# Kernel optimization log

Hardware: AMD Instinct MI355X
Metric: run time of the kernel (lower is better)

## Reference

```python
import jax, jax.numpy as jnp
import numpy as np

B, N, D = 2, 1024, 128
MID, OUT = 128, 128
DE, DG = 16, 64
MLP_SIZES = [32, 64, 64, OUT]  # hardcoded in the original module


def _lin_init(key, fan_in, fan_out):
    s = 1.0 / np.sqrt(fan_in)
    return jax.random.uniform(key, (fan_in, fan_out), jnp.float32, -s, s)


def setup_inputs() -> dict:
    key = jax.random.key(0)
    ks = jax.random.split(key, 16)
    inp = {
        "features": jax.random.normal(ks[0], (B, N, D), jnp.float32),
        "e_features": jax.random.normal(ks[1], (B, N, N, DE), jnp.float32),
        "g_features": jax.random.normal(ks[2], (B, DG), jnp.float32),
        "adj": (jax.random.uniform(ks[3], (B, N, N)) < 0.5).astype(jnp.float32),
        # message linears m_1, m_2 : D -> MID
        "w1": _lin_init(ks[4], D, MID), "b1": jnp.zeros((MID,), jnp.float32),
        "w2": _lin_init(ks[5], D, MID), "b2": jnp.zeros((MID,), jnp.float32),
        # output linear o1 : D -> OUT
        "wo": _lin_init(ks[6], D, OUT), "bo": jnp.zeros((OUT,), jnp.float32),
    }
    # MLP([32,64,64,OUT]) acting on MID-dim msgs
    sizes = [MID] + MLP_SIZES
    for i in range(4):
        inp[f"wm{i}"] = _lin_init(ks[7 + i], sizes[i], sizes[i + 1])
        inp[f"bm{i}"] = jnp.zeros((sizes[i + 1],), jnp.float32)
    return inp


def reference(features, e_features, g_features, adj,
              w1, b1, w2, b2, wo, bo,
              wm0, bm0, wm1, bm1, wm2, bm2, wm3, bm3):
    # e_features and g_features are shape-checked but unused by the original.
    msg_1 = features @ w1 + b1                      # (b, n, mid)
    msg_2 = features @ w2 + b2                      # (b, n, mid)
    # all-pairs broadcast-add: (b,1,n,mid) + (b,n,1,mid) -> (b,n,n,mid)
    msgs = msg_1[:, None, :, :] + msg_2[:, :, None, :]
    # masked max-reduce over sender axis (axis=1), default reduction=jnp.max
    msgs = jnp.max(msgs * adj[..., None], axis=1)   # (b, n, mid)
    h_1 = features @ wo + bo                        # (b, n, out)
    # hk.nets.MLP([32,64,64,out]): relu between layers, none at the end
    x = jax.nn.relu(msgs)
    x = jax.nn.relu(x @ wm0 + bm0)
    x = jax.nn.relu(x @ wm1 + bm1)
    x = jax.nn.relu(x @ wm2 + bm2)
    h_2 = x @ wm3 + bm3                             # (b, n, out)
    return h_1 + h_2
```

## Files before the change

kernel.cpp:

```cpp
#include <hip/hip_runtime.h>

#define NN 1024
#define NROWS 2048

#define NEG_INF (-__builtin_huge_valf())

__device__ __forceinline__ float orf(float v, unsigned int m) {
    return __uint_as_float(__float_as_uint(v) | m);
}

__global__ __launch_bounds__(256) void k1_msg2(
    const float* __restrict__ feat, const float* __restrict__ w2,
    const float* __restrict__ b2, float* __restrict__ msg2)
{
    __shared__ float sf[4][128];
    const int tid = threadIdx.x;
    const int rb = blockIdx.x * 4;
    if (tid < 128) {
        int r = tid >> 5, c = (tid & 31) * 4;
        *reinterpret_cast<float4*>(&sf[r][c]) =
            *reinterpret_cast<const float4*>(feat + (size_t)(rb + r)*128 + c);
    }
    __syncthreads();
    const int m = tid & 127, rh = tid >> 7;
    float a0 = 0.f, a1 = 0.f;
    #pragma unroll 4
    for (int k = 0; k < 128; ++k) {
        float wv = w2[k*128 + m];
        a0 = fmaf(sf[rh*2][k],   wv, a0);
        a1 = fmaf(sf[rh*2+1][k], wv, a1);
    }
    const float bb = b2[m];
    msg2[(size_t)(rb + rh*2)*128 + m]     = a0 + bb;
    msg2[(size_t)(rb + rh*2 + 1)*128 + m] = a1 + bb;
}

struct K2S {
    union {
        float scratch[8][16][132];
        struct { float sf[8][128];
                 float sx[8][128];
                 float sh0[8][32]; float sh1[8][64]; float sh2[8][64]; } c;
    } u;
    unsigned long long adjm[128];
    float m1[8][128];
    float hh[8][128];
};

__global__ __launch_bounds__(512) void k2_fused(
    const float* __restrict__ feat, const float* __restrict__ adj,
    const float* __restrict__ msg2,
    const float* __restrict__ w1, const float* __restrict__ b1,
    const float* __restrict__ wo, const float* __restrict__ bo,
    const float* __restrict__ wm0, const float* __restrict__ bm0,
    const float* __restrict__ wm1, const float* __restrict__ bm1,
    const float* __restrict__ wm2, const float* __restrict__ bm2,
    const float* __restrict__ wm3, const float* __restrict__ bm3,
    float* __restrict__ out)
{
    __shared__ K2S sh;
    const int tid = threadIdx.x;
    const int orig = (blockIdx.x & 7) * 32 + (blockIdx.x >> 3);
    const int b  = orig >> 7;
    const int j0 = (orig & 127) * 8;
    const int rb = b * NN + j0;

    if (tid < 256) {
        int r = tid >> 5, c = (tid & 31) * 4;
        *reinterpret_cast<float4*>(&sh.u.c.sf[r][c]) =
            *reinterpret_cast<const float4*>(feat + (size_t)(rb + r)*128 + c);
    }
    const float* ga = adj + (size_t)b*NN*NN + j0;
    float av[16];
    #pragma unroll
    for (int k = 0; k < 16; ++k) {
        int e = tid + k*512;
        av[k] = ga[(size_t)(e >> 3)*NN + (e & 7)];
    }
    __syncthreads();

    {
        const int m = tid & 127, rr = tid >> 7;
        float a1v[2] = {0,0}, aov[2] = {0,0};
        #pragma unroll 4
        for (int k = 0; k < 128; ++k) {
            float wv1 = w1[k*128 + m], wvo = wo[k*128 + m];
            #pragma unroll
            for (int r = 0; r < 2; ++r) {
                float f = sh.u.c.sf[rr*2 + r][k];
                a1v[r] = fmaf(f, wv1, a1v[r]);
                aov[r] = fmaf(f, wvo, aov[r]);
            }
        }
        const float bb1 = b1[m], bbo = bo[m];
        #pragma unroll
        for (int r = 0; r < 2; ++r) {
            sh.m1[rr*2 + r][m] = a1v[r] + bb1;
            sh.hh[rr*2 + r][m] = aov[r] + bbo;
        }
    }
    #pragma unroll
    for (int k = 0; k < 16; ++k) {
        unsigned long long bal = __ballot(av[k] != 0.f);
        if ((tid & 63) == 0) sh.adjm[(tid + k*512) >> 6] = bal;
    }
    __syncthreads();

    const int mq = tid & 31;
    const int s  = tid >> 5;
    const float* gmb = msg2 + ((size_t)b*NN)*128 + mq*4;
    const int ib = s * 64;

    float acc[8][4];
    #pragma unroll
    for (int j = 0; j < 8; ++j)
        #pragma unroll
        for (int w = 0; w < 4; ++w) acc[j][w] = NEG_INF;

    float4 v0 = *reinterpret_cast<const float4*>(gmb + (size_t)ib*128);
    float4 v1 = *reinterpret_cast<const float4*>(gmb + (size_t)(ib+1)*128);
    #pragma unroll 4
    for (int p = 0; p < 32; ++p) {
        float4 n0, n1;
        if (p < 31) {
            n0 = *reinterpret_cast<const float4*>(gmb + (size_t)(ib + 2*p + 2)*128);
            n1 = *reinterpret_cast<const float4*>(gmb + (size_t)(ib + 2*p + 3)*128);
        }
        const int i = ib + 2*p;
        unsigned long long word = sh.adjm[i >> 3];
        unsigned int b0 = (unsigned int)(word >> (((2*p)  & 7) * 8)) & 0xFFu;
        unsigned int b1 = (unsigned int)(word >> (((2*p+1)& 7) * 8)) & 0xFFu;
        const float* f0 = reinterpret_cast<const float*>(&v0);
        const float* f1 = reinterpret_cast<const float*>(&v1);
        #pragma unroll
        for (int j = 0; j < 8; ++j) {
            unsigned int k0 = (((b0 >> j) & 1u) - 1u) & 0xFFC00000u;
            unsigned int k1 = (((b1 >> j) & 1u) - 1u) & 0xFFC00000u;
            #pragma unroll
            for (int w = 0; w < 4; ++w) {
                acc[j][w] = fmaxf(fmaxf(acc[j][w], orf(f0[w], k0)), orf(f1[w], k1));
            }
        }
        v0 = n0; v1 = n1;
    }

    #pragma unroll
    for (int j = 0; j < 8; ++j)
        *reinterpret_cast<float4*>(&sh.u.scratch[j][s][mq*4]) =
            make_float4(acc[j][0], acc[j][1], acc[j][2], acc[j][3]);
    __syncthreads();
    float val0, val1;
    {
        int e0 = tid, e1 = tid + 512;
        int ja = e0 >> 7, ma = e0 & 127;
        int jb = e1 >> 7, mb = e1 & 127;
        float x = NEG_INF, y = NEG_INF;
        #pragma unroll
        for (int t = 0; t < 16; ++t) {
            x = fmaxf(x, sh.u.scratch[ja][t][ma]);
            y = fmaxf(y, sh.u.scratch[jb][t][mb]);
        }
        val0 = fmaxf(sh.m1[ja][ma] + x, 0.f);
        val1 = fmaxf(sh.m1[jb][mb] + y, 0.f);
    }
    __syncthreads();
    sh.u.c.sx[tid >> 7][tid & 127] = val0;
    sh.u.c.sx[(tid + 512) >> 7][(tid + 512) & 127] = val1;
    __syncthreads();

    if (tid < 256) {
        int r = tid >> 5, c = tid & 31;
        float a = bm0[c];
        #pragma unroll 8
        for (int k = 0; k < 128; ++k) a = fmaf(sh.u.c.sx[r][k], wm0[k*32 + c], a);
        sh.u.c.sh0[r][c] = fmaxf(a, 0.f);
    }
    __syncthreads();
    {
        int r = tid >> 6, c = tid & 63;
        float a = bm1[c];
        #pragma unroll
        for (int k = 0; k < 32; ++k) a = fmaf(sh.u.c.sh0[r][k], wm1[k*64 + c], a);
        sh.u.c.sh1[r][c] = fmaxf(a, 0.f);
    }
    __syncthreads();
    {
        int r = tid >> 6, c = tid & 63;
        float a = bm2[c];
        #pragma unroll 8
        for (int k = 0; k < 64; ++k) a = fmaf(sh.u.c.sh1[r][k], wm2[k*64 + c], a);
        sh.u.c.sh2[r][c] = fmaxf(a, 0.f);
    }
    __syncthreads();
    {
        int r2 = tid >> 7, c = tid & 127;
        float a0 = bm3[c], a1 = bm3[c];
        #pragma unroll 8
        for (int k = 0; k < 64; ++k) {
            float w = wm3[k*128 + c];
            a0 = fmaf(sh.u.c.sh2[r2][k],     w, a0);
            a1 = fmaf(sh.u.c.sh2[r2 + 4][k], w, a1);
        }
        out[(size_t)(rb + r2)*128 + c]     = sh.hh[r2][c]     + a0;
        out[(size_t)(rb + r2 + 4)*128 + c] = sh.hh[r2 + 4][c] + a1;
    }
}

extern "C" void kernel_launch(void* const* d_in, const int* in_sizes, int n_in,
                              void* d_out, int out_size, void* d_ws, size_t ws_size,
                              hipStream_t stream)
{
    const float* feat = (const float*)d_in[0];
    const float* adj  = (const float*)d_in[3];
    const float* w1 = (const float*)d_in[4];   const float* b1 = (const float*)d_in[5];
    const float* w2 = (const float*)d_in[6];   const float* b2 = (const float*)d_in[7];
    const float* wo = (const float*)d_in[8];   const float* bo = (const float*)d_in[9];
    const float* wm0 = (const float*)d_in[10]; const float* bm0 = (const float*)d_in[11];
    const float* wm1 = (const float*)d_in[12]; const float* bm1 = (const float*)d_in[13];
    const float* wm2 = (const float*)d_in[14]; const float* bm2 = (const float*)d_in[15];
    const float* wm3 = (const float*)d_in[16]; const float* bm3 = (const float*)d_in[17];
    float* out = (float*)d_out;

    float* msg2 = (float*)d_ws;

    k1_msg2<<<512, 256, 0, stream>>>(feat, w2, b2, msg2);

    k2_fused<<<256, 512, 0, stream>>>(feat, adj, msg2,
        w1, b1, wo, bo, wm0, bm0, wm1, bm1, wm2, bm2, wm3, bm3, out);
}
```

Measured before the change: 41.78 us.

## Move all three input linears into first kernel and precompute adjacency masks in LDS

The w1 and wo projections move out of the fused max-reduce kernel into the first kernel, which now computes msg1, msg2 and h1 together and writes them to workspace. This shortens the serial prologue of the main kernel. The main kernel also stores adjacency as precomputed 32-bit OR-masks in shared memory, replacing the ballot bit-packing and per-element bit extraction. In exchange there are extra global writes and reads for msg1 and h1, a larger LDS footprint for the mask array, and an added barrier before the scratch area is reused.

```diff
diff --git a/kernel.cpp b/kernel.cpp
--- a/kernel.cpp
+++ b/kernel.cpp
@@ -9,9 +9,12 @@
     return __uint_as_float(__float_as_uint(v) | m);
 }
 
-__global__ __launch_bounds__(256) void k1_msg2(
-    const float* __restrict__ feat, const float* __restrict__ w2,
-    const float* __restrict__ b2, float* __restrict__ msg2)
+__global__ __launch_bounds__(256) void k1_lin3(
+    const float* __restrict__ feat,
+    const float* __restrict__ w1, const float* __restrict__ b1,
+    const float* __restrict__ w2, const float* __restrict__ b2,
+    const float* __restrict__ wo, const float* __restrict__ bo,
+    float* __restrict__ msg1, float* __restrict__ msg2, float* __restrict__ h1)
 {
     __shared__ float sf[4][128];
     const int tid = threadIdx.x;
@@ -19,39 +22,44 @@
     if (tid < 128) {
         int r = tid >> 5, c = (tid & 31) * 4;
         *reinterpret_cast<float4*>(&sf[r][c]) =
-            *reinterpret_cast<const float4*>(feat + (size_t)(rb + r)*128 + c);
+            *reinterpret_cast<const float4*>(feat + (size_t)(rb + r) * 128 + c);
     }
     __syncthreads();
     const int m = tid & 127, rh = tid >> 7;
-    float a0 = 0.f, a1 = 0.f;
+    float a1[2] = {0,0}, a2[2] = {0,0}, ao[2] = {0,0};
     #pragma unroll 4
     for (int k = 0; k < 128; ++k) {
-        float wv = w2[k*128 + m];
-        a0 = fmaf(sf[rh*2][k],   wv, a0);
-        a1 = fmaf(sf[rh*2+1][k], wv, a1);
-    }
-    const float bb = b2[m];
-    msg2[(size_t)(rb + rh*2)*128 + m]     = a0 + bb;
-    msg2[(size_t)(rb + rh*2 + 1)*128 + m] = a1 + bb;
+        float wv1 = w1[k*128 + m], wv2 = w2[k*128 + m], wvo = wo[k*128 + m];
+        #pragma unroll
+        for (int r = 0; r < 2; ++r) {
+            float f = sf[rh*2 + r][k];
+            a1[r] = fmaf(f, wv1, a1[r]);
+            a2[r] = fmaf(f, wv2, a2[r]);
+            ao[r] = fmaf(f, wvo, ao[r]);
+        }
+    }
+    const float bb1 = b1[m], bb2 = b2[m], bbo = bo[m];
+    #pragma unroll
+    for (int r = 0; r < 2; ++r) {
+        size_t row = rb + rh*2 + r;
+        msg1[row*128 + m] = a1[r] + bb1;
+        msg2[row*128 + m] = a2[r] + bb2;
+        h1  [row*128 + m] = ao[r] + bbo;
+    }
 }
 
 struct K2S {
     union {
-        float scratch[8][16][132];
-        struct { float sf[8][128];
-                 float sx[8][128];
-                 float sh0[8][32]; float sh1[8][64]; float sh2[8][64]; } c;
+        float scratch[8][16][128];
+        unsigned int adjp[512][8][2];
+        struct { float sx[8][128]; float sh0[8][32];
+                 float sh1[8][64]; float sh2[8][64]; } c;
     } u;
-    unsigned long long adjm[128];
-    float m1[8][128];
-    float hh[8][128];
 };
 
 __global__ __launch_bounds__(512) void k2_fused(
-    const float* __restrict__ feat, const float* __restrict__ adj,
-    const float* __restrict__ msg2,
-    const float* __restrict__ w1, const float* __restrict__ b1,
-    const float* __restrict__ wo, const float* __restrict__ bo,
+    const float* __restrict__ adj, const float* __restrict__ msg2,
+    const float* __restrict__ msg1, const float* __restrict__ h1v,
     const float* __restrict__ wm0, const float* __restrict__ bm0,
     const float* __restrict__ wm1, const float* __restrict__ bm1,
     const float* __restrict__ wm2, const float* __restrict__ bm2,
@@ -65,11 +73,6 @@
     const int j0 = (orig & 127) * 8;
     const int rb = b * NN + j0;
 
-    if (tid < 256) {
-        int r = tid >> 5, c = (tid & 31) * 4;
-        *reinterpret_cast<float4*>(&sh.u.c.sf[r][c]) =
-            *reinterpret_cast<const float4*>(feat + (size_t)(rb + r)*128 + c);
-    }
     const float* ga = adj + (size_t)b*NN*NN + j0;
     float av[16];
     #pragma unroll
@@ -77,32 +80,13 @@
         int e = tid + k*512;
         av[k] = ga[(size_t)(e >> 3)*NN + (e & 7)];
     }
-    __syncthreads();
-
-    {
-        const int m = tid & 127, rr = tid >> 7;
-        float a1v[2] = {0,0}, aov[2] = {0,0};
-        #pragma unroll 4
-        for (int k = 0; k < 128; ++k) {
-            float wv1 = w1[k*128 + m], wvo = wo[k*128 + m];
-            #pragma unroll
-            for (int r = 0; r < 2; ++r) {
-                float f = sh.u.c.sf[rr*2 + r][k];
-                a1v[r] = fmaf(f, wv1, a1v[r]);
-                aov[r] = fmaf(f, wvo, aov[r]);
-            }
-        }
-        const float bb1 = b1[m], bbo = bo[m];
-        #pragma unroll
-        for (int r = 0; r < 2; ++r) {
-            sh.m1[rr*2 + r][m] = a1v[r] + bb1;
-            sh.hh[rr*2 + r][m] = aov[r] + bbo;
-        }
-    }
+    unsigned int* ap = &sh.u.adjp[0][0][0];
     #pragma unroll
     for (int k = 0; k < 16; ++k) {
-        unsigned long long bal = __ballot(av[k] != 0.f);
-        if ((tid & 63) == 0) sh.adjm[(tid + k*512) >> 6] = bal;
+        int e = tid + k*512;
+        int i = e >> 3, jl = e & 7;
+        ap[(size_t)(i >> 1)*16 + jl*2 + (i & 1)] =
+            (av[k] != 0.f) ? 0u : 0xFFC00000u;
     }
     __syncthreads();
 
@@ -126,16 +110,16 @@
             n0 = *reinterpret_cast<const float4*>(gmb + (size_t)(ib + 2*p + 2)*128);
             n1 = *reinterpret_cast<const float4*>(gmb + (size_t)(ib + 2*p + 3)*128);
         }
-        const int i = ib + 2*p;
-        unsigned long long word = sh.adjm[i >> 3];
-        unsigned int b0 = (unsigned int)(word >> (((2*p)  & 7) * 8)) & 0xFFu;
-        unsigned int b1 = (unsigned int)(word >> (((2*p+1)& 7) * 8)) & 0xFFu;
+        const int pg = s*32 + p;
+        const uint4* mr = reinterpret_cast<const uint4*>(ap + (size_t)pg*16);
+        uint4 q0 = mr[0], q1 = mr[1], q2 = mr[2], q3 = mr[3];
+        unsigned int kk[16] = {q0.x,q0.y,q0.z,q0.w, q1.x,q1.y,q1.z,q1.w,
+                               q2.x,q2.y,q2.z,q2.w, q3.x,q3.y,q3.z,q3.w};
         const float* f0 = reinterpret_cast<const float*>(&v0);
         const float* f1 = reinterpret_cast<const float*>(&v1);
         #pragma unroll
         for (int j = 0; j < 8; ++j) {
-            unsigned int k0 = (((b0 >> j) & 1u) - 1u) & 0xFFC00000u;
-            unsigned int k1 = (((b1 >> j) & 1u) - 1u) & 0xFFC00000u;
+            unsigned int k0 = kk[2*j], k1 = kk[2*j + 1];
             #pragma unroll
             for (int w = 0; w < 4; ++w) {
                 acc[j][w] = fmaxf(fmaxf(acc[j][w], orf(f0[w], k0)), orf(f1[w], k1));
@@ -144,6 +128,7 @@
         v0 = n0; v1 = n1;
     }
 
+    __syncthreads();
     #pragma unroll
     for (int j = 0; j < 8; ++j)
         *reinterpret_cast<float4*>(&sh.u.scratch[j][s][mq*4]) =
@@ -160,8 +145,8 @@
             x = fmaxf(x, sh.u.scratch[ja][t][ma]);
             y = fmaxf(y, sh.u.scratch[jb][t][mb]);
         }
-        val0 = fmaxf(sh.m1[ja][ma] + x, 0.f);
-        val1 = fmaxf(sh.m1[jb][mb] + y, 0.f);
+        val0 = fmaxf(msg1[(size_t)(rb + ja)*128 + ma] + x, 0.f);
+        val1 = fmaxf(msg1[(size_t)(rb + jb)*128 + mb] + y, 0.f);
     }
     __syncthreads();
     sh.u.c.sx[tid >> 7][tid & 127] = val0;
@@ -201,8 +186,8 @@
             a0 = fmaf(sh.u.c.sh2[r2][k],     w, a0);
             a1 = fmaf(sh.u.c.sh2[r2 + 4][k], w, a1);
         }
-        out[(size_t)(rb + r2)*128 + c]     = sh.hh[r2][c]     + a0;
-        out[(size_t)(rb + r2 + 4)*128 + c] = sh.hh[r2 + 4][c] + a1;
+        out[(size_t)(rb + r2)*128 + c]     = h1v[(size_t)(rb + r2)*128 + c]     + a0;
+        out[(size_t)(rb + r2 + 4)*128 + c] = h1v[(size_t)(rb + r2 + 4)*128 + c] + a1;
     }
 }
 
@@ -221,10 +206,13 @@
     const float* wm3 = (const float*)d_in[16]; const float* bm3 = (const float*)d_in[17];
     float* out = (float*)d_out;
 
-    float* msg2 = (float*)d_ws;
-
-    k1_msg2<<<512, 256, 0, stream>>>(feat, w2, b2, msg2);
-
-    k2_fused<<<256, 512, 0, stream>>>(feat, adj, msg2,
-        w1, b1, wo, bo, wm0, bm0, wm1, bm1, wm2, bm2, wm3, bm3, out);
-}
+    const size_t MAT = (size_t)NROWS * 128;
+    float* msg1 = (float*)d_ws;
+    float* msg2 = msg1 + MAT;
+    float* h1v  = msg1 + 2*MAT;
+
+    k1_lin3<<<512, 256, 0, stream>>>(feat, w1, b1, w2, b2, wo, bo, msg1, msg2, h1v);
+
+    k2_fused<<<256, 512, 0, stream>>>(adj, msg2, msg1, h1v,
+        wm0, bm0, wm1, bm1, wm2, bm2, wm3, bm3, out);
+}
```

Result: faster. 36.47 us, median of 2 (-12.7%).

## Precompute per-element adjacency masks in LDS and deepen msg2 prefetch

Applied to the files above, without the earlier changes.

Replaces the ballot-packed adjacency bitmask with a per-element 32-bit OR-mask array stored in shared memory. The hot max loop then loads ready masks with uint4 LDS reads instead of extracting bits with shifts, and one barrier is removed. The msg2 prefetch is deepened to two row pairs ahead. k1 also gets a remapped block order so that row ranges match k2's XCD-interleaved blocks. The cost is 64KB of LDS for the mask array, reused through a union with scratch, which may reduce occupancy.

```diff
diff --git a/kernel.cpp b/kernel.cpp
--- a/kernel.cpp
+++ b/kernel.cpp
@@ -15,7 +15,9 @@
 {
     __shared__ float sf[4][128];
     const int tid = threadIdx.x;
-    const int rb = blockIdx.x * 4;
+    const int k = blockIdx.x;
+    const int x = k & 7, t = k >> 3;
+    const int rb = ((x >> 2) << 10) + ((x & 3) << 8) + (t << 2);
     if (tid < 128) {
         int r = tid >> 5, c = (tid & 31) * 4;
         *reinterpret_cast<float4*>(&sf[r][c]) =
@@ -25,10 +27,10 @@
     const int m = tid & 127, rh = tid >> 7;
     float a0 = 0.f, a1 = 0.f;
     #pragma unroll 4
-    for (int k = 0; k < 128; ++k) {
-        float wv = w2[k*128 + m];
-        a0 = fmaf(sf[rh*2][k],   wv, a0);
-        a1 = fmaf(sf[rh*2+1][k], wv, a1);
+    for (int kk = 0; kk < 128; ++kk) {
+        float wv = w2[kk*128 + m];
+        a0 = fmaf(sf[rh*2][kk],   wv, a0);
+        a1 = fmaf(sf[rh*2+1][kk], wv, a1);
     }
     const float bb = b2[m];
     msg2[(size_t)(rb + rh*2)*128 + m]     = a0 + bb;
@@ -37,14 +39,14 @@
 
 struct K2S {
     union {
-        float scratch[8][16][132];
-        struct { float sf[8][128];
-                 float sx[8][128];
-                 float sh0[8][32]; float sh1[8][64]; float sh2[8][64]; } c;
+        float scratch[8][16][128];
+        unsigned int adjp[512][8][2];
+        struct { float sx[8][128]; float sh0[8][32];
+                 float sh1[8][64]; float sh2[8][64]; } c;
     } u;
-    unsigned long long adjm[128];
     float m1[8][128];
     float hh[8][128];
+    float sfeat[8][128];
 };
 
 __global__ __launch_bounds__(512) void k2_fused(
@@ -67,7 +69,7 @@
 
     if (tid < 256) {
         int r = tid >> 5, c = (tid & 31) * 4;
-        *reinterpret_cast<float4*>(&sh.u.c.sf[r][c]) =
+        *reinterpret_cast<float4*>(&sh.sfeat[r][c]) =
             *reinterpret_cast<const float4*>(feat + (size_t)(rb + r)*128 + c);
     }
     const float* ga = adj + (size_t)b*NN*NN + j0;
@@ -76,6 +78,14 @@
     for (int k = 0; k < 16; ++k) {
         int e = tid + k*512;
         av[k] = ga[(size_t)(e >> 3)*NN + (e & 7)];
+    }
+    unsigned int* ap = &sh.u.adjp[0][0][0];
+    #pragma unroll
+    for (int k = 0; k < 16; ++k) {
+        int e = tid + k*512;
+        int i = e >> 3, jl = e & 7;
+        ap[(size_t)(i >> 1)*16 + jl*2 + (i & 1)] =
+            (av[k] != 0.f) ? 0u : 0xFFC00000u;
     }
     __syncthreads();
 
@@ -87,7 +97,7 @@
             float wv1 = w1[k*128 + m], wvo = wo[k*128 + m];
             #pragma unroll
             for (int r = 0; r < 2; ++r) {
-                float f = sh.u.c.sf[rr*2 + r][k];
+                float f = sh.sfeat[rr*2 + r][k];
                 a1v[r] = fmaf(f, wv1, a1v[r]);
                 aov[r] = fmaf(f, wvo, aov[r]);
             }
@@ -99,12 +109,6 @@
             sh.hh[rr*2 + r][m] = aov[r] + bbo;
         }
     }
-    #pragma unroll
-    for (int k = 0; k < 16; ++k) {
-        unsigned long long bal = __ballot(av[k] != 0.f);
-        if ((tid & 63) == 0) sh.adjm[(tid + k*512) >> 6] = bal;
-    }
-    __syncthreads();
 
     const int mq = tid & 31;
     const int s  = tid >> 5;
@@ -117,33 +121,36 @@
         #pragma unroll
         for (int w = 0; w < 4; ++w) acc[j][w] = NEG_INF;
 
-    float4 v0 = *reinterpret_cast<const float4*>(gmb + (size_t)ib*128);
-    float4 v1 = *reinterpret_cast<const float4*>(gmb + (size_t)(ib+1)*128);
+    float4 a0 = *reinterpret_cast<const float4*>(gmb + (size_t)(ib+0)*128);
+    float4 a1 = *reinterpret_cast<const float4*>(gmb + (size_t)(ib+1)*128);
+    float4 c0 = *reinterpret_cast<const float4*>(gmb + (size_t)(ib+2)*128);
+    float4 c1 = *reinterpret_cast<const float4*>(gmb + (size_t)(ib+3)*128);
     #pragma unroll 4
     for (int p = 0; p < 32; ++p) {
         float4 n0, n1;
-        if (p < 31) {
-            n0 = *reinterpret_cast<const float4*>(gmb + (size_t)(ib + 2*p + 2)*128);
-            n1 = *reinterpret_cast<const float4*>(gmb + (size_t)(ib + 2*p + 3)*128);
-        }
-        const int i = ib + 2*p;
-        unsigned long long word = sh.adjm[i >> 3];
-        unsigned int b0 = (unsigned int)(word >> (((2*p)  & 7) * 8)) & 0xFFu;
-        unsigned int b1 = (unsigned int)(word >> (((2*p+1)& 7) * 8)) & 0xFFu;
-        const float* f0 = reinterpret_cast<const float*>(&v0);
-        const float* f1 = reinterpret_cast<const float*>(&v1);
+        if (p < 30) {
+            n0 = *reinterpret_cast<const float4*>(gmb + (size_t)(ib + 2*p + 4)*128);
+            n1 = *reinterpret_cast<const float4*>(gmb + (size_t)(ib + 2*p + 5)*128);
+        }
+        const int pg = s*32 + p;
+        const uint4* mr = reinterpret_cast<const uint4*>(ap + (size_t)pg*16);
+        uint4 q0 = mr[0], q1 = mr[1], q2 = mr[2], q3 = mr[3];
+        unsigned int kk[16] = {q0.x,q0.y,q0.z,q0.w, q1.x,q1.y,q1.z,q1.w,
+                               q2.x,q2.y,q2.z,q2.w, q3.x,q3.y,q3.z,q3.w};
+        const float* f0 = reinterpret_cast<const float*>(&a0);
+        const float* f1 = reinterpret_cast<const float*>(&a1);
         #pragma unroll
         for (int j = 0; j < 8; ++j) {
-            unsigned int k0 = (((b0 >> j) & 1u) - 1u) & 0xFFC00000u;
-            unsigned int k1 = (((b1 >> j) & 1u) - 1u) & 0xFFC00000u;
+            unsigned int k0 = kk[2*j], k1 = kk[2*j + 1];
             #pragma unroll
             for (int w = 0; w < 4; ++w) {
                 acc[j][w] = fmaxf(fmaxf(acc[j][w], orf(f0[w], k0)), orf(f1[w], k1));
             }
         }
-        v0 = n0; v1 = n1;
-    }
-
+        a0 = c0; a1 = c1; c0 = n0; c1 = n1;
+    }
+
+    __syncthreads();
     #pragma unroll
     for (int j = 0; j < 8; ++j)
         *reinterpret_cast<float4*>(&sh.u.scratch[j][s][mq*4]) =
@@ -194,15 +201,15 @@
     __syncthreads();
     {
         int r2 = tid >> 7, c = tid & 127;
-        float a0 = bm3[c], a1 = bm3[c];
+        float a0_ = bm3[c], a1_ = bm3[c];
         #pragma unroll 8
         for (int k = 0; k < 64; ++k) {
             float w = wm3[k*128 + c];
-            a0 = fmaf(sh.u.c.sh2[r2][k],     w, a0);
-            a1 = fmaf(sh.u.c.sh2[r2 + 4][k], w, a1);
-        }
-        out[(size_t)(rb + r2)*128 + c]     = sh.hh[r2][c]     + a0;
-        out[(size_t)(rb + r2 + 4)*128 + c] = sh.hh[r2 + 4][c] + a1;
+            a0_ = fmaf(sh.u.c.sh2[r2][k],     w, a0_);
+            a1_ = fmaf(sh.u.c.sh2[r2 + 4][k], w, a1_);
+        }
+        out[(size_t)(rb + r2)*128 + c]     = sh.hh[r2][c]     + a0_;
+        out[(size_t)(rb + r2 + 4)*128 + c] = sh.hh[r2 + 4][c] + a1_;
     }
 }
 
```

New measurement: 38.55 us. 7.7% less time.
